# Performance work log

Measured on AMD Instinct MI355X. Metric: run time of the kernel, lower is better.

## Reference

```python
import jax, jax.numpy as jnp
import numpy as np

DIM = 256
HEADS = 8
WS = 16      # window size
WN = 16      # num windows (img 64x64)
KS = 3
B = 16
IMG = 64


def setup_inputs() -> dict:
    key = jax.random.key(0)
    ks = jax.random.split(key, 12)
    d = DIM
    hid = d // 16  # SE hidden (d >= 64)
    inp = {
        "x": jax.random.normal(ks[0], (B, d, IMG, IMG), dtype=jnp.float32),
        "conv_w": jax.random.normal(ks[1], (WN, d, d, KS, KS), dtype=jnp.float32) * 0.02,
        "wqkv": jax.random.normal(ks[2], (d, 3 * d), dtype=jnp.float32) * 0.02,
        "bqkv": jax.random.normal(ks[3], (3 * d,), dtype=jnp.float32) * 0.02,
        "wout": jax.random.normal(ks[4], (d, d), dtype=jnp.float32) * 0.02,
        "bout": jax.random.normal(ks[5], (d,), dtype=jnp.float32) * 0.02,
        "se_w1": jax.random.normal(ks[6], (WN, hid, d), dtype=jnp.float32) * 0.05,
        "se_b1": jax.random.normal(ks[7], (WN, hid), dtype=jnp.float32) * 0.02,
        "se_w2": jax.random.normal(ks[8], (WN, d, hid), dtype=jnp.float32) * 0.05,
        "se_b2": jax.random.normal(ks[9], (WN, d), dtype=jnp.float32) * 0.02,
        "ln_g": jnp.ones((d,), dtype=jnp.float32),
        "ln_b": jnp.zeros((d,), dtype=jnp.float32),
    }
    return inp


def reference(x, conv_w, wqkv, bqkv, wout, bout, se_w1, se_b1, se_w2, se_b2, ln_g, ln_b):
    Bn, C, H, W = x.shape
    hd = C // HEADS
    scale = hd ** (-0.5)

    # window partition: (WN, B, C, WS, WS), windows in (h_idx, w_idx) row-major order
    xw = x.reshape(Bn, C, H // WS, WS, W // WS, WS).transpose(2, 4, 0, 1, 3, 5)
    xw = xw.reshape(WN, Bn, C, WS, WS)

    # kernel tokens: per-layer weight.view(B, C, -1).permute(0,2,1), cat on axis 1
    last = C * KS * KS // Bn
    kt = conv_w.reshape(WN, Bn, C, last).transpose(1, 0, 3, 2).reshape(Bn, WN * last, C)

    # self-attention over kernel tokens (batch axis becomes dim C after reshape)
    qkv = kt @ wqkv + bqkv                                    # (B, WN*last, 3C)
    qkv = qkv.reshape(C, WN * KS * KS, 3, HEADS, hd).transpose(2, 0, 3, 1, 4)
    q, k, v = qkv[0] * scale, qkv[1], qkv[2]                  # (C, H, T, hd), T = WN*KS*KS
    attn = jax.nn.softmax(jnp.einsum('dhqe,dhke->dhqk', q, k), axis=-1)
    o = jnp.einsum('dhqk,dhke->dhqe', attn, v)
    o = o.transpose(0, 2, 1, 3).reshape(C, WN * KS * KS, C)
    o = o @ wout + bout
    kern = o.reshape(C, WN, KS, KS, C).transpose(1, 0, 4, 2, 3)  # (WN, Cout, Cin, KS, KS)

    # SE gating per window: kernels[i] treated as (batch=C, channels=C, KS, KS)
    pooled = kern.mean(axis=(3, 4))                            # (WN, C, C)
    h = jax.nn.relu(jnp.einsum('wbc,whc->wbh', pooled, se_w1) + se_b1[:, None, :])
    s = jax.nn.sigmoid(jnp.einsum('wbh,wch->wbc', h, se_w2) + se_b2[:, None, :])
    kern = kern * s[:, :, :, None, None]

    # per-window conv as a single grouped conv (groups = WN)
    xg = xw.transpose(1, 0, 2, 3, 4).reshape(Bn, WN * C, WS, WS)
    wg = kern.reshape(WN * C, C, KS, KS)
    yg = jax.lax.conv_general_dilated(xg, wg, (1, 1), ((1, 1), (1, 1)),
                                      feature_group_count=WN)
    yw = yg.reshape(Bn, WN, C, WS, WS).transpose(1, 0, 2, 3, 4)  # (WN, B, C, WS, WS)

    # window reverse
    y = yw.reshape(H // WS, W // WS, Bn, C, WS, WS).transpose(2, 3, 0, 4, 1, 5)
    y = y.reshape(Bn, C, H, W)

    # channel layernorm (eps=1e-5) + residual
    yn = y.transpose(0, 2, 3, 1)
    mu = yn.mean(-1, keepdims=True)
    var = ((yn - mu) ** 2).mean(-1, keepdims=True)
    yn = (yn - mu) / jnp.sqrt(var + 1e-5) * ln_g + ln_b
    return x + yn.transpose(0, 3, 1, 2)
```

## Files before the change

kernel.cpp:

```cpp
#include <hip/hip_runtime.h>

typedef __bf16 bf16;
typedef __bf16 bf16x8 __attribute__((ext_vector_type(8)));
typedef _Float16 f16;
typedef _Float16 f16x8 __attribute__((ext_vector_type(8)));
typedef float f32x4 __attribute__((ext_vector_type(4)));

#define SCALE_Q 0.17677669529663687f
#define KSCALE 64.0f
#define KSCALE_INV 0.015625f

__global__ __launch_bounds__(256) void k_prep_w(const float* __restrict__ wqkv,
                                                const float* __restrict__ wout,
                                                bf16* __restrict__ wqkv_t,
                                                f16* __restrict__ wout_h,
                                                f16* __restrict__ wout_l) {
    int n = blockIdx.x, k = threadIdx.x;
    if (n < 768) {
        wqkv_t[n * 256 + k] = (bf16)wqkv[k * 768 + n];
    } else {
        float f = wout[k * 256 + (n - 768)] * KSCALE;
        f16 hi = (f16)f;
        wout_h[(n - 768) * 256 + k] = hi;
        wout_l[(n - 768) * 256 + k] = (f16)(f - (float)hi);
    }
}

__global__ __launch_bounds__(256) void k_build_kt(const float* __restrict__ conv_w,
                                                  bf16* __restrict__ kt) {
    __shared__ float lds[16 * 145];
    int w = blockIdx.x >> 8, co = blockIdx.x & 255;
    const float* src = conv_w + (size_t)(w * 256 + co) * 2304;
    for (int i = threadIdx.x; i < 2304; i += 256) {
        int m = i / 144, tt = i - m * 144;
        lds[m * 145 + tt] = src[i];
    }
    __syncthreads();
    int b = co >> 4, c0 = (co & 15) << 4;
    size_t rbase = (size_t)(b * 16 + w) * 144;
    for (int i = threadIdx.x; i < 2304; i += 256) {
        int t = i >> 4, m = i & 15;
        kt[(rbase + t) * 256 + c0 + m] = (bf16)lds[m * 145 + t];
    }
}

typedef const __attribute__((address_space(1))) unsigned int* gas_t;
typedef __attribute__((address_space(3))) unsigned int* las_t;

__device__ __forceinline__ void async_copy16(const void* g, void* l) {
    __builtin_amdgcn_global_load_lds((gas_t)g, (las_t)l, 16, 0, 0);
}

__device__ __forceinline__ void mfma_tile_bf16(const bf16* As, const bf16* Bs,
                                               f32x4 acc[4][4]) {
    int lane = threadIdx.x & 63;
    int wave = threadIdx.x >> 6;
    int wm = (wave >> 1) * 64, wn = (wave & 1) * 64;
    int lrow = lane & 15, quad = lane >> 4;
    bf16x8 af[4], bfr[4];
#pragma unroll
    for (int i = 0; i < 4; i++) {
        int r = wm + i * 16 + lrow;
        af[i] = *(const bf16x8*)(As + r * 32 + ((quad ^ ((r >> 1) & 3)) << 3));
        int n = wn + i * 16 + lrow;
        bfr[i] = *(const bf16x8*)(Bs + n * 32 + ((quad ^ ((n >> 1) & 3)) << 3));
    }
#pragma unroll
    for (int i = 0; i < 4; i++)
#pragma unroll
        for (int j = 0; j < 4; j++)
            acc[i][j] = __builtin_amdgcn_mfma_f32_16x16x32_bf16(af[i], bfr[j], acc[i][j], 0, 0, 0);
}

__device__ __forceinline__ void mfma_tile_f16_dual(const f16* As, const f16* Bhs,
                                                   const f16* Bls, f32x4 acc[4][4]) {
    int lane = threadIdx.x & 63;
    int wave = threadIdx.x >> 6;
    int wm = (wave >> 1) * 64, wn = (wave & 1) * 64;
    int lrow = lane & 15, quad = lane >> 4;
    f16x8 af[4], bh[4], bl[4];
#pragma unroll
    for (int i = 0; i < 4; i++) {
        int r = wm + i * 16 + lrow;
        af[i] = *(const f16x8*)(As + r * 32 + ((quad ^ ((r >> 1) & 3)) << 3));
        int n = wn + i * 16 + lrow;
        bh[i] = *(const f16x8*)(Bhs + n * 32 + ((quad ^ ((n >> 1) & 3)) << 3));
        bl[i] = *(const f16x8*)(Bls + n * 32 + ((quad ^ ((n >> 1) & 3)) << 3));
    }
#pragma unroll
    for (int i = 0; i < 4; i++)
#pragma unroll
        for (int j = 0; j < 4; j++) {
            acc[i][j] = __builtin_amdgcn_mfma_f32_16x16x32_f16(af[i], bh[j], acc[i][j], 0, 0, 0);
            acc[i][j] = __builtin_amdgcn_mfma_f32_16x16x32_f16(af[i], bl[j], acc[i][j], 0, 0, 0);
        }
}

__device__ __forceinline__ void mfma_tile_f16_dual8(const f16* As, const f16* Bhs,
                                                    const f16* Bls, f32x4 acc[8][4]) {
    int lane = threadIdx.x & 63;
    int wave = threadIdx.x >> 6;
    int wm = (wave >> 1) * 128, wn = (wave & 1) * 64;
    int lrow = lane & 15, quad = lane >> 4;
    f16x8 af[8], bh[4], bl[4];
#pragma unroll
    for (int i = 0; i < 8; i++) {
        int r = wm + i * 16 + lrow;
        af[i] = *(const f16x8*)(As + r * 32 + ((quad ^ ((r >> 1) & 3)) << 3));
    }
#pragma unroll
    for (int j = 0; j < 4; j++) {
        int n = wn + j * 16 + lrow;
        bh[j] = *(const f16x8*)(Bhs + n * 32 + ((quad ^ ((n >> 1) & 3)) << 3));
        bl[j] = *(const f16x8*)(Bls + n * 32 + ((quad ^ ((n >> 1) & 3)) << 3));
    }
#pragma unroll
    for (int i = 0; i < 8; i++)
#pragma unroll
        for (int j = 0; j < 4; j++) {
            acc[i][j] = __builtin_amdgcn_mfma_f32_16x16x32_f16(af[i], bh[j], acc[i][j], 0, 0, 0);
            acc[i][j] = __builtin_amdgcn_mfma_f32_16x16x32_f16(af[i], bl[j], acc[i][j], 0, 0, 0);
        }
}

__global__ __launch_bounds__(256) void k_gemm_qkv(const bf16* __restrict__ A,
                                                  const bf16* __restrict__ Bt,
                                                  const float* __restrict__ bias,
                                                  bf16* __restrict__ outb,
                                                  int N, int K) {
    __shared__ __align__(16) bf16 As[2][128 * 32];
    __shared__ __align__(16) bf16 Bs[2][128 * 32];
    int m0 = blockIdx.y * 128, n0 = blockIdx.x * 128;
    int t = threadIdx.x, wave = t >> 6, lane = t & 63;
    int chunk0 = wave * 2, chunk1 = chunk0 + 1;
    int row0 = chunk0 * 16 + (lane >> 2), row1 = row0 + 16;
    int sw = ((lane & 3) ^ ((row0 >> 1) & 3)) << 3;
    const unsigned short* Ag = (const unsigned short*)A;
    const unsigned short* Bg = (const unsigned short*)Bt;
    size_t a0 = (size_t)(m0 + row0) * K + sw, a1 = (size_t)(m0 + row1) * K + sw;
    size_t b0 = (size_t)(n0 + row0) * K + sw, b1 = (size_t)(n0 + row1) * K + sw;
    f32x4 acc[4][4] = {};
#define STG_QKV(cur, k0)                                        \
    async_copy16(Ag + a0 + (k0), &As[cur][chunk0 * 512]);       \
    async_copy16(Ag + a1 + (k0), &As[cur][chunk1 * 512]);       \
    async_copy16(Bg + b0 + (k0), &Bs[cur][chunk0 * 512]);       \
    async_copy16(Bg + b1 + (k0), &Bs[cur][chunk1 * 512]);
    STG_QKV(0, 0);
    int cur = 0, NT = K >> 5;
#pragma unroll 1
    for (int it = 0; it < NT; it++) {
        if (it < NT - 1) {
            STG_QKV(cur ^ 1, (it + 1) << 5);
            asm volatile("s_waitcnt vmcnt(4)" ::: "memory");
        } else {
            asm volatile("s_waitcnt vmcnt(0)" ::: "memory");
        }
        __builtin_amdgcn_s_barrier();
        mfma_tile_bf16(As[cur], Bs[cur], acc);
        asm volatile("s_waitcnt lgkmcnt(0)" ::: "memory");
        __builtin_amdgcn_s_barrier();
        cur ^= 1;
    }
#undef STG_QKV
    int wm = (wave >> 1) * 64, wn = (wave & 1) * 64;
    int lrow = lane & 15, quad = lane >> 4;
#pragma unroll
    for (int i = 0; i < 4; i++)
#pragma unroll
        for (int j = 0; j < 4; j++) {
            int col = n0 + wn + j * 16 + lrow;
            float bv = bias[col];
#pragma unroll
            for (int rr = 0; rr < 4; rr++) {
                int row = m0 + wm + i * 16 + quad * 4 + rr;
                float v = acc[i][j][rr] + bv;
                if (col < 256) v *= SCALE_Q;
                outb[(size_t)row * N + col] = (bf16)v;
            }
        }
}

__global__ __launch_bounds__(256) void k_gemm_split2(const f16* __restrict__ Ag_,
                                                     const f16* __restrict__ Bhg,
                                                     const f16* __restrict__ Blg,
                                                     const float* __restrict__ bias,
                                                     float* __restrict__ outf,
                                                     int N, int K) {
    __shared__ __align__(16) f16 As[2][128 * 32];
    __shared__ __align__(16) f16 Bh[2][128 * 32];
    __shared__ __align__(16) f16 Bl[2][128 * 32];
    int m0 = blockIdx.y * 128, n0 = blockIdx.x * 128;
    int t = threadIdx.x, wave = t >> 6, lane = t & 63;
    int chunk0 = wave * 2, chunk1 = chunk0 + 1;
    int row0 = chunk0 * 16 + (lane >> 2), row1 = row0 + 16;
    int sw = ((lane & 3) ^ ((row0 >> 1) & 3)) << 3;
    const unsigned short* Au = (const unsigned short*)Ag_;
    const unsigned short* Bhu = (const unsigned short*)Bhg;
    const unsigned short* Blu = (const unsigned short*)Blg;
    size_t a0 = (size_t)(m0 + row0) * K + sw, a1 = (size_t)(m0 + row1) * K + sw;
    size_t b0 = (size_t)(n0 + row0) * K + sw, b1 = (size_t)(n0 + row1) * K + sw;
    f32x4 acc[4][4] = {};
#define STG_SP2(cur, k0)                                        \
    async_copy16(Au + a0 + (k0), &As[cur][chunk0 * 512]);       \
    async_copy16(Au + a1 + (k0), &As[cur][chunk1 * 512]);       \
    async_copy16(Bhu + b0 + (k0), &Bh[cur][chunk0 * 512]);      \
    async_copy16(Bhu + b1 + (k0), &Bh[cur][chunk1 * 512]);      \
    async_copy16(Blu + b0 + (k0), &Bl[cur][chunk0 * 512]);      \
    async_copy16(Blu + b1 + (k0), &Bl[cur][chunk1 * 512]);
    STG_SP2(0, 0);
    int cur = 0, NT = K >> 5;
#pragma unroll 1
    for (int it = 0; it < NT; it++) {
        if (it < NT - 1) {
            STG_SP2(cur ^ 1, (it + 1) << 5);
            asm volatile("s_waitcnt vmcnt(6)" ::: "memory");
        } else {
            asm volatile("s_waitcnt vmcnt(0)" ::: "memory");
        }
        __builtin_amdgcn_s_barrier();
        mfma_tile_f16_dual(As[cur], Bh[cur], Bl[cur], acc);
        asm volatile("s_waitcnt lgkmcnt(0)" ::: "memory");
        __builtin_amdgcn_s_barrier();
        cur ^= 1;
    }
#undef STG_SP2
    int wm = (wave >> 1) * 64, wn = (wave & 1) * 64;
    int lrow = lane & 15, quad = lane >> 4;
#pragma unroll
    for (int i = 0; i < 4; i++)
#pragma unroll
        for (int j = 0; j < 4; j++) {
            int col = n0 + wn + j * 16 + lrow;
            float bv = bias[col];
#pragma unroll
            for (int rr = 0; rr < 4; rr++) {
                int row = m0 + wm + i * 16 + quad * 4 + rr;
                outf[(size_t)row * N + col] = acc[i][j][rr] * KSCALE_INV + bv;
            }
        }
}

__global__ __launch_bounds__(256) void k_attn(const bf16* __restrict__ qkv,
                                              f16* __restrict__ o16) {
    __shared__ bf16 Qs[144 * 32];
    __shared__ bf16 Ks[144 * 32];
    __shared__ f16 Vt[32 * 160];
    __shared__ f16 Ps[4 * 16 * 168];
    int d = blockIdx.x >> 3, h = blockIdx.x & 7;
    const bf16* base = qkv + (size_t)d * 144 * 768 + h * 32;
    int t = threadIdx.x;

    for (int i = t; i < 512; i += 256) Vt[(i >> 4) * 160 + 144 + (i & 15)] = (f16)0.f;
    for (int i = t; i < 576; i += 256) {
        int row = i >> 2, part = i & 3;
        const bf16* rp = base + (size_t)row * 768;
        uint4 vq = *(const uint4*)(rp + (part << 3));
        uint4 vk = *(const uint4*)(rp + 256 + (part << 3));
        int sw = ((part ^ (row & 3)) << 3);
        *(uint4*)(Qs + row * 32 + sw) = vq;
        *(uint4*)(Ks + row * 32 + sw) = vk;
        bf16x8 v8 = *(const bf16x8*)(rp + 512 + (part << 3));
#pragma unroll
        for (int j = 0; j < 8; j++) Vt[(part * 8 + j) * 160 + row] = (f16)(float)v8[j];
    }
    __syncthreads();

    int wave = t >> 6, lane = t & 63;
    int lrow = lane & 15, quad = lane >> 4;
    f16* Pw = Ps + wave * 16 * 168;
    for (int i = lane; i < 256; i += 64) Pw[(i >> 4) * 168 + 144 + (i & 15)] = (f16)0.f;

    bf16x8 kf[9];
#pragma unroll
    for (int nt = 0; nt < 9; nt++) {
        int r = nt * 16 + lrow;
        kf[nt] = *(const bf16x8*)(Ks + r * 32 + ((quad ^ (r & 3)) << 3));
    }

    for (int mt = wave; mt < 9; mt += 4) {
        int qr = mt * 16 + lrow;
        bf16x8 qf = *(const bf16x8*)(Qs + qr * 32 + ((quad ^ (qr & 3)) << 3));
        f32x4 s[9];
#pragma unroll
        for (int nt = 0; nt < 9; nt++) {
            f32x4 z = {0.f, 0.f, 0.f, 0.f};
            s[nt] = __builtin_amdgcn_mfma_f32_16x16x32_bf16(qf, kf[nt], z, 0, 0, 0);
        }
        f32x4 mx = s[0];
#pragma unroll
        for (int nt = 1; nt < 9; nt++)
#pragma unroll
            for (int c = 0; c < 4; c++) mx[c] = fmaxf(mx[c], s[nt][c]);
#pragma unroll
        for (int off = 1; off < 16; off <<= 1)
#pragma unroll
            for (int c = 0; c < 4; c++) mx[c] = fmaxf(mx[c], __shfl_xor(mx[c], off));
        f32x4 sm = {0.f, 0.f, 0.f, 0.f};
#pragma unroll
        for (int nt = 0; nt < 9; nt++)
#pragma unroll
            for (int c = 0; c < 4; c++) {
                float e = __expf(s[nt][c] - mx[c]);
                s[nt][c] = e;
                sm[c] += e;
            }
#pragma unroll
        for (int off = 1; off < 16; off <<= 1)
#pragma unroll
            for (int c = 0; c < 4; c++) sm[c] += __shfl_xor(sm[c], off);
        f32x4 inv;
#pragma unroll
        for (int c = 0; c < 4; c++) inv[c] = 1.f / sm[c];
#pragma unroll
        for (int nt = 0; nt < 9; nt++)
#pragma unroll
            for (int c = 0; c < 4; c++)
                Pw[(quad * 4 + c) * 168 + nt * 16 + lrow] = (f16)(s[nt][c] * inv[c]);

        f32x4 o0 = {0.f, 0.f, 0.f, 0.f}, o1 = {0.f, 0.f, 0.f, 0.f};
#pragma unroll
        for (int kt = 0; kt < 5; kt++) {
            f16x8 pf = *(const f16x8*)(Pw + lrow * 168 + kt * 32 + quad * 8);
            f16x8 v0 = *(const f16x8*)(Vt + lrow * 160 + kt * 32 + quad * 8);
            f16x8 v1 = *(const f16x8*)(Vt + (16 + lrow) * 160 + kt * 32 + quad * 8);
            o0 = __builtin_amdgcn_mfma_f32_16x16x32_f16(pf, v0, o0, 0, 0, 0);
            o1 = __builtin_amdgcn_mfma_f32_16x16x32_f16(pf, v1, o1, 0, 0, 0);
        }
        size_t ro = ((size_t)d * 144 + mt * 16) * 256 + h * 32;
#pragma unroll
        for (int c = 0; c < 4; c++) {
            size_t rr = ro + (size_t)(quad * 4 + c) * 256;
            o16[rr + lrow] = (f16)o0[c];
            o16[rr + 16 + lrow] = (f16)o1[c];
        }
    }
}

__global__ __launch_bounds__(256) void k_se_scale(const float* __restrict__ kern,
                                                  const float* __restrict__ w1,
                                                  const float* __restrict__ b1,
                                                  const float* __restrict__ w2,
                                                  const float* __restrict__ b2,
                                                  f16* __restrict__ kern_hi,
                                                  f16* __restrict__ kern_lo) {
    __shared__ float pooled[256];
    __shared__ float hbuf[16];
    int w = blockIdx.x >> 8, Co = blockIdx.x & 255;
    int ci = threadIdx.x;
    const float* kb = kern + (size_t)(Co * 16 + w) * 9 * 256;
    float v9[9];
    float pv = 0.f;
#pragma unroll
    for (int k9 = 0; k9 < 9; k9++) { v9[k9] = kb[k9 * 256 + ci]; pv += v9[k9]; }
    pooled[ci] = pv * (1.f / 9.f);
    __syncthreads();
    {
        int hid = ci >> 4, l16 = ci & 15;
        const float* w1p = w1 + (size_t)(w * 16 + hid) * 256;
        float hs = 0.f;
#pragma unroll
        for (int c = l16; c < 256; c += 16) hs += pooled[c] * w1p[c];
        hs += __shfl_xor(hs, 1);
        hs += __shfl_xor(hs, 2);
        hs += __shfl_xor(hs, 4);
        hs += __shfl_xor(hs, 8);
        if (l16 == 0) hbuf[hid] = fmaxf(hs + b1[w * 16 + hid], 0.f);
    }
    __syncthreads();
    const float* w2p = w2 + (size_t)(w * 256 + ci) * 16;
    float ss = b2[w * 256 + ci];
#pragma unroll
    for (int j = 0; j < 16; j++) ss += hbuf[j] * w2p[j];
    float s = (1.f / (1.f + __expf(-ss))) * KSCALE;
    size_t outo = (size_t)(w * 256 + Co) * 2304;
    f16* khi = kern_hi + outo;
    f16* klo = kern_lo + outo;
#pragma unroll
    for (int k9 = 0; k9 < 9; k9++) {
        float f = v9[k9] * s;
        f16 hi = (f16)f;
        khi[k9 * 256 + ci] = hi;
        klo[k9 * 256 + ci] = (f16)(f - (float)hi);
    }
}

__global__ __launch_bounds__(256) void k_zero_pad(f16* __restrict__ xcl) {
    int wb = blockIdx.x;
    f16* base = xcl + (size_t)wb * 18 * 18 * 256;
    int ci = threadIdx.x;
#pragma unroll 1
    for (int i = 0; i < 68; i++) {
        int py, px;
        if (i < 18) { py = 0; px = i; }
        else if (i < 36) { py = 17; px = i - 18; }
        else { int k = i - 36; py = 1 + (k >> 1); px = (k & 1) * 17; }
        base[((size_t)py * 18 + px) * 256 + ci] = (f16)0.f;
    }
}

__global__ __launch_bounds__(256) void k_fill_xcl(const float* __restrict__ x,
                                                  f16* __restrict__ xcl) {
    int bx = blockIdx.x;
    int b = bx >> 6, gy = bx & 63;
    int wrow = gy >> 4, py = gy & 15;
    int ci = threadIdx.x;
    const float* xp = x + ((size_t)(b * 256 + ci) * 64 + gy) * 64;
    for (int wx = 0; wx < 4; wx++) {
        int w = wrow * 4 + wx;
        size_t o = (((size_t)(w * 16 + b) * 18 + py + 1) * 18 + 1) * 256 + ci;
#pragma unroll
        for (int px = 0; px < 16; px++)
            xcl[o + (size_t)px * 256] = (f16)xp[wx * 16 + px];
    }
}

__global__ __launch_bounds__(256, 2) void k_conv_gemm(const f16* __restrict__ xcl,
                                                      const f16* __restrict__ kern_hi,
                                                      const f16* __restrict__ kern_lo,
                                                      float* __restrict__ y) {
    __shared__ __align__(16) f16 As[2][256 * 32];
    __shared__ __align__(16) f16 Bh[2][128 * 32];
    __shared__ __align__(16) f16 Bl[2][128 * 32];
    int f = blockIdx.x;
    int xcd = f & 7, i5 = f >> 3;
    int w = xcd * 2 + (i5 >> 5);
    int rem = i5 & 31;
    int by = rem >> 1;
    int n0 = (rem & 1) * 128;
    int m0 = by * 256;
    const unsigned short* xw = (const unsigned short*)(xcl + (size_t)w * 16 * 18 * 18 * 256);
    const unsigned short* Bthu = (const unsigned short*)(kern_hi + (size_t)w * 256 * 2304);
    const unsigned short* Btlu = (const unsigned short*)(kern_lo + (size_t)w * 256 * 2304);
    int t = threadIdx.x, wave = t >> 6, lane = t & 63;
    int sw = ((lane & 3) ^ ((lane >> 3) & 3)) << 3;
    size_t aA[4];
#pragma unroll
    for (int c = 0; c < 4; c++) {
        int row = (wave * 4 + c) * 16 + (lane >> 2);
        int py = row >> 4, px = row & 15;
        aA[c] = ((size_t)(by * 18 + py) * 18 + px) * 256 + sw;
    }
    int rb0 = (wave * 2) * 16 + (lane >> 2), rb1 = rb0 + 16;
    size_t bB0 = (size_t)(n0 + rb0) * 2304 + sw;
    size_t bB1 = (size_t)(n0 + rb1) * 2304 + sw;
    f32x4 acc[8][4] = {};
#define STG_CONV(cur, k0)                                                      \
    {                                                                          \
        int k9_ = (k0) >> 8;                                                   \
        int koff_ = ((k9_ / 3) * 18 + (k9_ % 3)) * 256 + ((k0) & 255);         \
        async_copy16(xw + aA[0] + koff_, &As[cur][(wave * 4 + 0) * 512]);      \
        async_copy16(xw + aA[1] + koff_, &As[cur][(wave * 4 + 1) * 512]);      \
        async_copy16(xw + aA[2] + koff_, &As[cur][(wave * 4 + 2) * 512]);      \
        async_copy16(xw + aA[3] + koff_, &As[cur][(wave * 4 + 3) * 512]);      \
        async_copy16(Bthu + bB0 + (k0), &Bh[cur][(wave * 2 + 0) * 512]);       \
        async_copy16(Bthu + bB1 + (k0), &Bh[cur][(wave * 2 + 1) * 512]);       \
        async_copy16(Btlu + bB0 + (k0), &Bl[cur][(wave * 2 + 0) * 512]);       \
        async_copy16(Btlu + bB1 + (k0), &Bl[cur][(wave * 2 + 1) * 512]);       \
    }
    STG_CONV(0, 0);
    int cur = 0;
#pragma unroll 1
    for (int it = 0; it < 72; it++) {
        if (it < 71) {
            STG_CONV(cur ^ 1, (it + 1) << 5);
            asm volatile("s_waitcnt vmcnt(8)" ::: "memory");
        } else {
            asm volatile("s_waitcnt vmcnt(0)" ::: "memory");
        }
        __builtin_amdgcn_s_barrier();
        mfma_tile_f16_dual8(As[cur], Bh[cur], Bl[cur], acc);
        asm volatile("s_waitcnt lgkmcnt(0)" ::: "memory");
        __builtin_amdgcn_s_barrier();
        cur ^= 1;
    }
#undef STG_CONV
    int lrow = lane & 15, quad = lane >> 4;
    int wm = (wave >> 1) * 128, wn = (wave & 1) * 64;
    float* yw = y + (size_t)w * 4096 * 256;
#pragma unroll
    for (int i = 0; i < 8; i++)
#pragma unroll
        for (int j = 0; j < 4; j++) {
            int col = n0 + wn + j * 16 + lrow;
#pragma unroll
            for (int rr = 0; rr < 4; rr++) {
                int row = m0 + wm + i * 16 + quad * 4 + rr;
                yw[(size_t)row * 256 + col] = acc[i][j][rr] * KSCALE_INV;
            }
        }
}

__global__ __launch_bounds__(256) void k_ln_res(const float* __restrict__ y,
                                                const float* __restrict__ x,
                                                const float* __restrict__ g,
                                                const float* __restrict__ be,
                                                float* __restrict__ out) {
    __shared__ float vbuf[32 * 257];
    __shared__ float stats[32][2];
    int bx = blockIdx.x;
    int half = bx & 1, gy = (bx >> 1) & 63, b = bx >> 7;
    int t = threadIdx.x;
    int j = t >> 3, sub = t & 7;
    int gx = half * 32 + j;
    int w = (gy >> 4) * 4 + (gx >> 4);
    int p = (gy & 15) * 16 + (gx & 15);
    const float* yp = y + ((size_t)w * 4096 + b * 256 + p) * 256 + sub * 32;
    float sum = 0.f, sq = 0.f;
#pragma unroll
    for (int c = 0; c < 32; c++) {
        float v = yp[c];
        vbuf[j * 257 + sub * 32 + c] = v;
        sum += v; sq += v * v;
    }
    sum += __shfl_xor(sum, 1); sq += __shfl_xor(sq, 1);
    sum += __shfl_xor(sum, 2); sq += __shfl_xor(sq, 2);
    sum += __shfl_xor(sum, 4); sq += __shfl_xor(sq, 4);
    if (sub == 0) {
        float mean = sum * (1.f / 256.f);
        float var = sq * (1.f / 256.f) - mean * mean;
        stats[j][0] = mean;
        stats[j][1] = rsqrtf(var + 1e-5f);
    }
    __syncthreads();
    int wv = t >> 6, lane = t & 63;
    int chp = lane >> 5, lgx = lane & 31;
    float mu = stats[lgx][0], rstd = stats[lgx][1];
    const float* xrow = x + ((size_t)(b * 256) * 64 + gy) * 64 + half * 32 + lgx;
    float* orow = out + ((size_t)(b * 256) * 64 + gy) * 64 + half * 32 + lgx;
#pragma unroll 4
    for (int it = 0; it < 32; it++) {
        int ch = wv * 64 + it * 2 + chp;
        float v = vbuf[lgx * 257 + ch];
        float r = (v - mu) * rstd * g[ch] + be[ch] + xrow[(size_t)ch * 4096];
        orow[(size_t)ch * 4096] = r;
    }
}

extern "C" void kernel_launch(void* const* d_in, const int* in_sizes, int n_in,
                              void* d_out, int out_size, void* d_ws, size_t ws_size,
                              hipStream_t stream) {
    const float* x      = (const float*)d_in[0];
    const float* conv_w = (const float*)d_in[1];
    const float* wqkv   = (const float*)d_in[2];
    const float* bqkv   = (const float*)d_in[3];
    const float* wout   = (const float*)d_in[4];
    const float* bout   = (const float*)d_in[5];
    const float* se_w1  = (const float*)d_in[6];
    const float* se_b1  = (const float*)d_in[7];
    const float* se_w2  = (const float*)d_in[8];
    const float* se_b2  = (const float*)d_in[9];
    const float* ln_g   = (const float*)d_in[10];
    const float* ln_b   = (const float*)d_in[11];
    float* out = (float*)d_out;

    char* ws = (char*)d_ws;
    bf16*  kt      = (bf16*)(ws + 0);
    f16*   o16     = (f16*)(ws + 0);
    f16*   kern_hi = (f16*)(ws + 0);
    f16*   kern_lo = (f16*)(ws + 18874368);
    bf16*  wqkv_t  = (bf16*)(ws + 37748736);
    f16*   wout_h  = (f16*)(ws + 38141952);
    f16*   wout_l  = (f16*)(ws + 38273024);
    f16*   xcl     = (f16*)(ws + 38404096);
    bf16*  qkv     = (bf16*)(ws + 80871424);
    float* kern_f  = (float*)(ws + 80871424);
    float* y       = (float*)(ws + 80871424);

    k_prep_w<<<1024, 256, 0, stream>>>(wqkv, wout, wqkv_t, wout_h, wout_l);
    k_build_kt<<<4096, 256, 0, stream>>>(conv_w, kt);
    k_gemm_qkv<<<dim3(6, 288), 256, 0, stream>>>(kt, wqkv_t, bqkv, qkv, 768, 256);
    k_attn<<<2048, 256, 0, stream>>>(qkv, o16);
    k_gemm_split2<<<dim3(2, 288), 256, 0, stream>>>(o16, wout_h, wout_l, bout, kern_f, 256, 256);
    k_se_scale<<<4096, 256, 0, stream>>>(kern_f, se_w1, se_b1, se_w2, se_b2, kern_hi, kern_lo);
    k_zero_pad<<<256, 256, 0, stream>>>(xcl);
    k_fill_xcl<<<1024, 256, 0, stream>>>(x, xcl);
    k_conv_gemm<<<512, 256, 0, stream>>>(xcl, kern_hi, kern_lo, y);
    k_ln_res<<<2048, 256, 0, stream>>>(y, x, ln_g, ln_b, out);
}
```

Baseline: 474.1 us.

## Fuse channel layernorm and residual into conv GEMM epilogue with full-N tiles

Widens the conv GEMM block to 512 threads covering all 256 output channels, so each block holds complete channel rows for its 256 pixels. Layernorm statistics are then reduced in the epilogue through shuffles and shared memory, and the normalized result plus residual is written straight to the output. This removes the fp32 intermediate y and the separate layernorm kernel, at the cost of larger shared memory (~100KB), only 256 blocks, and strided, poorly coalesced output stores in NCHW.

```diff
diff --git a/kernel.cpp b/kernel.cpp
--- a/kernel.cpp
+++ b/kernel.cpp
@@ -96,11 +96,11 @@
         }
 }
 
-__device__ __forceinline__ void mfma_tile_f16_dual8(const f16* As, const f16* Bhs,
-                                                    const f16* Bls, f32x4 acc[8][4]) {
+__device__ __forceinline__ void mfma_tile_f16_dual8b(const f16* As, const f16* Bhs,
+                                                     const f16* Bls, f32x4 acc[8][4]) {
     int lane = threadIdx.x & 63;
     int wave = threadIdx.x >> 6;
-    int wm = (wave >> 1) * 128, wn = (wave & 1) * 64;
+    int wm = (wave >> 2) * 128, wn = (wave & 3) * 64;
     int lrow = lane & 15, quad = lane >> 4;
     f16x8 af[8], bh[4], bl[4];
 #pragma unroll
@@ -414,48 +414,46 @@
     }
 }
 
-__global__ __launch_bounds__(256, 2) void k_conv_gemm(const f16* __restrict__ xcl,
-                                                      const f16* __restrict__ kern_hi,
-                                                      const f16* __restrict__ kern_lo,
-                                                      float* __restrict__ y) {
+__global__ __launch_bounds__(512, 2) void k_conv_ln(const f16* __restrict__ xcl,
+                                                    const f16* __restrict__ kern_hi,
+                                                    const f16* __restrict__ kern_lo,
+                                                    const float* __restrict__ x,
+                                                    const float* __restrict__ g,
+                                                    const float* __restrict__ be,
+                                                    float* __restrict__ out) {
     __shared__ __align__(16) f16 As[2][256 * 32];
-    __shared__ __align__(16) f16 Bh[2][128 * 32];
-    __shared__ __align__(16) f16 Bl[2][128 * 32];
+    __shared__ __align__(16) f16 Bh[2][256 * 32];
+    __shared__ __align__(16) f16 Bl[2][256 * 32];
+    __shared__ float part[256][4][2];
+    __shared__ float stats[256][2];
     int f = blockIdx.x;
-    int xcd = f & 7, i5 = f >> 3;
-    int w = xcd * 2 + (i5 >> 5);
-    int rem = i5 & 31;
-    int by = rem >> 1;
-    int n0 = (rem & 1) * 128;
-    int m0 = by * 256;
+    int xcd = f & 7, i8 = f >> 3;
+    int w = xcd * 2 + (i8 >> 4);
+    int by = i8 & 15;
     const unsigned short* xw = (const unsigned short*)(xcl + (size_t)w * 16 * 18 * 18 * 256);
     const unsigned short* Bthu = (const unsigned short*)(kern_hi + (size_t)w * 256 * 2304);
     const unsigned short* Btlu = (const unsigned short*)(kern_lo + (size_t)w * 256 * 2304);
     int t = threadIdx.x, wave = t >> 6, lane = t & 63;
-    int sw = ((lane & 3) ^ ((lane >> 3) & 3)) << 3;
-    size_t aA[4];
-#pragma unroll
-    for (int c = 0; c < 4; c++) {
-        int row = (wave * 4 + c) * 16 + (lane >> 2);
+    int sw = ((t & 3) ^ ((t >> 3) & 3)) << 3;
+    size_t aA[2], bB[2];
+#pragma unroll
+    for (int c = 0; c < 2; c++) {
+        int row = c * 128 + (t >> 2);
         int py = row >> 4, px = row & 15;
         aA[c] = ((size_t)(by * 18 + py) * 18 + px) * 256 + sw;
-    }
-    int rb0 = (wave * 2) * 16 + (lane >> 2), rb1 = rb0 + 16;
-    size_t bB0 = (size_t)(n0 + rb0) * 2304 + sw;
-    size_t bB1 = (size_t)(n0 + rb1) * 2304 + sw;
+        bB[c] = (size_t)row * 2304 + sw;
+    }
     f32x4 acc[8][4] = {};
-#define STG_CONV(cur, k0)                                                      \
-    {                                                                          \
-        int k9_ = (k0) >> 8;                                                   \
-        int koff_ = ((k9_ / 3) * 18 + (k9_ % 3)) * 256 + ((k0) & 255);         \
-        async_copy16(xw + aA[0] + koff_, &As[cur][(wave * 4 + 0) * 512]);      \
-        async_copy16(xw + aA[1] + koff_, &As[cur][(wave * 4 + 1) * 512]);      \
-        async_copy16(xw + aA[2] + koff_, &As[cur][(wave * 4 + 2) * 512]);      \
-        async_copy16(xw + aA[3] + koff_, &As[cur][(wave * 4 + 3) * 512]);      \
-        async_copy16(Bthu + bB0 + (k0), &Bh[cur][(wave * 2 + 0) * 512]);       \
-        async_copy16(Bthu + bB1 + (k0), &Bh[cur][(wave * 2 + 1) * 512]);       \
-        async_copy16(Btlu + bB0 + (k0), &Bl[cur][(wave * 2 + 0) * 512]);       \
-        async_copy16(Btlu + bB1 + (k0), &Bl[cur][(wave * 2 + 1) * 512]);       \
+#define STG_CONV(cur, k0)                                                        \
+    {                                                                            \
+        int k9_ = (k0) >> 8;                                                     \
+        int koff_ = ((k9_ / 3) * 18 + (k9_ % 3)) * 256 + ((k0) & 255);           \
+        async_copy16(xw + aA[0] + koff_, &As[cur][wave * 512]);                  \
+        async_copy16(xw + aA[1] + koff_, &As[cur][4096 + wave * 512]);           \
+        async_copy16(Bthu + bB[0] + (k0), &Bh[cur][wave * 512]);                 \
+        async_copy16(Bthu + bB[1] + (k0), &Bh[cur][4096 + wave * 512]);          \
+        async_copy16(Btlu + bB[0] + (k0), &Bl[cur][wave * 512]);                 \
+        async_copy16(Btlu + bB[1] + (k0), &Bl[cur][4096 + wave * 512]);          \
     }
     STG_CONV(0, 0);
     int cur = 0;
@@ -463,77 +461,72 @@
     for (int it = 0; it < 72; it++) {
         if (it < 71) {
             STG_CONV(cur ^ 1, (it + 1) << 5);
-            asm volatile("s_waitcnt vmcnt(8)" ::: "memory");
+            asm volatile("s_waitcnt vmcnt(6)" ::: "memory");
         } else {
             asm volatile("s_waitcnt vmcnt(0)" ::: "memory");
         }
         __builtin_amdgcn_s_barrier();
-        mfma_tile_f16_dual8(As[cur], Bh[cur], Bl[cur], acc);
+        mfma_tile_f16_dual8b(As[cur], Bh[cur], Bl[cur], acc);
         asm volatile("s_waitcnt lgkmcnt(0)" ::: "memory");
         __builtin_amdgcn_s_barrier();
         cur ^= 1;
     }
 #undef STG_CONV
     int lrow = lane & 15, quad = lane >> 4;
-    int wm = (wave >> 1) * 128, wn = (wave & 1) * 64;
-    float* yw = y + (size_t)w * 4096 * 256;
+    int wm = (wave >> 2) * 128, wn = (wave & 3) * 64;
 #pragma unroll
     for (int i = 0; i < 8; i++)
 #pragma unroll
-        for (int j = 0; j < 4; j++) {
-            int col = n0 + wn + j * 16 + lrow;
-#pragma unroll
-            for (int rr = 0; rr < 4; rr++) {
-                int row = m0 + wm + i * 16 + quad * 4 + rr;
-                yw[(size_t)row * 256 + col] = acc[i][j][rr] * KSCALE_INV;
+        for (int rr = 0; rr < 4; rr++) {
+            float s1 = 0.f, s2 = 0.f;
+#pragma unroll
+            for (int j = 0; j < 4; j++) {
+                float v = acc[i][j][rr] * KSCALE_INV;
+                s1 += v; s2 += v * v;
             }
-        }
-}
-
-__global__ __launch_bounds__(256) void k_ln_res(const float* __restrict__ y,
-                                                const float* __restrict__ x,
-                                                const float* __restrict__ g,
-                                                const float* __restrict__ be,
-                                                float* __restrict__ out) {
-    __shared__ float vbuf[32 * 257];
-    __shared__ float stats[32][2];
-    int bx = blockIdx.x;
-    int half = bx & 1, gy = (bx >> 1) & 63, b = bx >> 7;
-    int t = threadIdx.x;
-    int j = t >> 3, sub = t & 7;
-    int gx = half * 32 + j;
-    int w = (gy >> 4) * 4 + (gx >> 4);
-    int p = (gy & 15) * 16 + (gx & 15);
-    const float* yp = y + ((size_t)w * 4096 + b * 256 + p) * 256 + sub * 32;
-    float sum = 0.f, sq = 0.f;
-#pragma unroll
-    for (int c = 0; c < 32; c++) {
-        float v = yp[c];
-        vbuf[j * 257 + sub * 32 + c] = v;
-        sum += v; sq += v * v;
-    }
-    sum += __shfl_xor(sum, 1); sq += __shfl_xor(sq, 1);
-    sum += __shfl_xor(sum, 2); sq += __shfl_xor(sq, 2);
-    sum += __shfl_xor(sum, 4); sq += __shfl_xor(sq, 4);
-    if (sub == 0) {
-        float mean = sum * (1.f / 256.f);
-        float var = sq * (1.f / 256.f) - mean * mean;
-        stats[j][0] = mean;
-        stats[j][1] = rsqrtf(var + 1e-5f);
-    }
+            s1 += __shfl_xor(s1, 1); s2 += __shfl_xor(s2, 1);
+            s1 += __shfl_xor(s1, 2); s2 += __shfl_xor(s2, 2);
+            s1 += __shfl_xor(s1, 4); s2 += __shfl_xor(s2, 4);
+            s1 += __shfl_xor(s1, 8); s2 += __shfl_xor(s2, 8);
+            if (lrow == 0) {
+                int p = wm + i * 16 + quad * 4 + rr;
+                part[p][wave & 3][0] = s1;
+                part[p][wave & 3][1] = s2;
+            }
+        }
     __syncthreads();
-    int wv = t >> 6, lane = t & 63;
-    int chp = lane >> 5, lgx = lane & 31;
-    float mu = stats[lgx][0], rstd = stats[lgx][1];
-    const float* xrow = x + ((size_t)(b * 256) * 64 + gy) * 64 + half * 32 + lgx;
-    float* orow = out + ((size_t)(b * 256) * 64 + gy) * 64 + half * 32 + lgx;
-#pragma unroll 4
-    for (int it = 0; it < 32; it++) {
-        int ch = wv * 64 + it * 2 + chp;
-        float v = vbuf[lgx * 257 + ch];
-        float r = (v - mu) * rstd * g[ch] + be[ch] + xrow[(size_t)ch * 4096];
-        orow[(size_t)ch * 4096] = r;
-    }
+    if (t < 256) {
+        float s1 = part[t][0][0] + part[t][1][0] + part[t][2][0] + part[t][3][0];
+        float s2 = part[t][0][1] + part[t][1][1] + part[t][2][1] + part[t][3][1];
+        float mean = s1 * (1.f / 256.f);
+        float var = s2 * (1.f / 256.f) - mean * mean;
+        stats[t][0] = mean;
+        stats[t][1] = rsqrtf(var + 1e-5f);
+    }
+    __syncthreads();
+    float gv[4], bev[4];
+#pragma unroll
+    for (int j = 0; j < 4; j++) {
+        int cc = wn + j * 16 + lrow;
+        gv[j] = g[cc]; bev[j] = be[cc];
+    }
+    int gy0 = (w >> 2) * 16, gx0 = (w & 3) * 16;
+#pragma unroll
+    for (int i = 0; i < 8; i++)
+#pragma unroll
+        for (int rr = 0; rr < 4; rr++) {
+            int p = wm + i * 16 + quad * 4 + rr;
+            float mu = stats[p][0], rs = stats[p][1];
+            int gy = gy0 + (p >> 4), gx = gx0 + (p & 15);
+            size_t base = ((size_t)(by * 256) * 64 + gy) * 64 + gx;
+#pragma unroll
+            for (int j = 0; j < 4; j++) {
+                int cc = wn + j * 16 + lrow;
+                float v = acc[i][j][rr] * KSCALE_INV;
+                size_t a = base + (size_t)cc * 4096;
+                out[a] = (v - mu) * rs * gv[j] + bev[j] + x[a];
+            }
+        }
 }
 
 extern "C" void kernel_launch(void* const* d_in, const int* in_sizes, int n_in,
@@ -564,7 +557,6 @@
     f16*   xcl     = (f16*)(ws + 38404096);
     bf16*  qkv     = (bf16*)(ws + 80871424);
     float* kern_f  = (float*)(ws + 80871424);
-    float* y       = (float*)(ws + 80871424);
 
     k_prep_w<<<1024, 256, 0, stream>>>(wqkv, wout, wqkv_t, wout_h, wout_l);
     k_build_kt<<<4096, 256, 0, stream>>>(conv_w, kt);
@@ -574,6 +566,5 @@
     k_se_scale<<<4096, 256, 0, stream>>>(kern_f, se_w1, se_b1, se_w2, se_b2, kern_hi, kern_lo);
     k_zero_pad<<<256, 256, 0, stream>>>(xcl);
     k_fill_xcl<<<1024, 256, 0, stream>>>(x, xcl);
-    k_conv_gemm<<<512, 256, 0, stream>>>(xcl, kern_hi, kern_lo, y);
-    k_ln_res<<<2048, 256, 0, stream>>>(y, x, ln_g, ln_b, out);
-}
+    k_conv_ln<<<256, 512, 0, stream>>>(xcl, kern_hi, kern_lo, x, ln_g, ln_b, out);
+}
```

Result: slower. 494.8 us (+4.4%).
